# Optimization experiments

Measured on AMD Instinct MI355X. Metric: run time of the kernel, lower is better.

Reference implementation:

```python
import jax, jax.numpy as jnp
import numpy as np
import math

WINDOW_SIZE = 1024
CAUSAL = True


def setup_inputs() -> dict:
    key = jax.random.key(0)
    kq, kk, kv = jax.random.split(key, 3)
    B, H, L, D = 2, 16, 4096, 128
    q = jax.random.normal(kq, (B, H, L, D), dtype=jnp.float32)
    k = jax.random.normal(kk, (B, H, L, D), dtype=jnp.float32)
    v = jax.random.normal(kv, (B, H, L, D), dtype=jnp.float32)
    return {"q": q, "k": k, "v": v}


def _sliding_window_attention(q, k, v):
    # Faithful port of SlidingWindowAttention._blockwise_attention (L > 2048 path).
    B, H, L, D = q.shape
    block = min(WINDOW_SIZE, 1024)
    scale = 1.0 / math.sqrt(D)
    half_w = WINDOW_SIZE // 2
    outs = []
    # Python loop over a small fixed number of blocks (L/block = 4), not data dims.
    for s in range(0, L, block):
        e = min(s + block, L)
        ks = max(0, s - half_w)
        ke = min(L, e + half_w)
        if CAUSAL:
            ke = min(ke, e)
        qb = q[:, :, s:e, :]          # [B,H,Q,D]
        kb = k[:, :, ks:ke, :]        # [B,H,K,D]
        vb = v[:, :, ks:ke, :]        # [B,H,K,D]
        scores = jnp.einsum('bhqd,bhkd->bhqk', qb, kb) * scale
        if CAUSAL:
            qi = jnp.arange(s, e)[:, None]   # [Q,1]
            ki = jnp.arange(ks, ke)[None, :]  # [1,K]
            causal_mask = qi >= ki            # [Q,K]
            scores = jnp.where(causal_mask[None, None], scores, -jnp.inf)
        attn = jax.nn.softmax(scores, axis=-1)
        outs.append(jnp.einsum('bhqk,bhkd->bhqd', attn, vb))
    return jnp.concatenate(outs, axis=2)


def reference(q, k, v):
    return _sliding_window_attention(q, k, v)
```

## Files before the change

### kernel.cpp

```cpp
#include <hip/hip_runtime.h>
#include <hip/hip_bf16.h>

typedef __bf16 bf16_t;
typedef __bf16 bf16x8 __attribute__((ext_vector_type(8)));
typedef __bf16 bf16x4 __attribute__((ext_vector_type(4)));
typedef float f32x4 __attribute__((ext_vector_type(4)));

#define L_SEQ 4096
#define D_DIM 128
#define QT 64
#define KT 64
#define LDK 136
#define LDV 72
#define LDP 72

__global__ __launch_bounds__(256, 2)
void swa_fwd(const float* __restrict__ Qg,
             const float* __restrict__ Kg,
             const float* __restrict__ Vg,
             float* __restrict__ Og) {
    __shared__ __align__(16) bf16_t Kt[KT][LDK];
    __shared__ __align__(16) bf16_t Vt[D_DIM][LDV];
    __shared__ __align__(16) bf16_t Pst[4][16][LDP];

    const int t    = threadIdx.x;
    const int w    = t >> 6;
    const int ln   = t & 15;
    const int quad = (t & 63) >> 4;

    const int id = blockIdx.x;
    const int bh = id & 31;
    const int g  = id >> 5;
    const int q0 = g & 7;
    const int kk = g >> 3;
    const int qt = 16 * (kk >> 1) + ((kk & 1) ? (15 - q0) : q0);

    const size_t base = (size_t)bh * L_SEQ * D_DIM;
    const float* Qp = Qg + base;
    const float* Kp = Kg + base;
    const float* Vp = Vg + base;
    float*       Op = Og + base;

    const int qbase  = qt * QT;
    const int blk    = qbase & ~1023;
    const int kstart = (blk - 512) > 0 ? (blk - 512) : 0;
    const int kend   = qbase + QT;
    const int ntile  = (kend - kstart) / KT;

    const int qw = qbase + w * 16;

    const float SC  = 0.08838834764831845f * 1.4426950408889634f;
    const float FIX = 8.0f;

    bf16x8 qf[4];
    {
        const float* qrow = Qp + (size_t)(qw + ln) * D_DIM + quad * 8;
        #pragma unroll
        for (int ks = 0; ks < 4; ++ks) {
            f32x4 a = *(const f32x4*)(qrow + ks * 32);
            f32x4 b = *(const f32x4*)(qrow + ks * 32 + 4);
            bf16x8 q8;
            #pragma unroll
            for (int j = 0; j < 4; ++j) {
                q8[j]     = (bf16_t)(a[j] * SC);
                q8[4 + j] = (bf16_t)(b[j] * SC);
            }
            qf[ks] = q8;
        }
    }

    f32x4 Oacc[8];
    #pragma unroll
    for (int dt = 0; dt < 8; ++dt) Oacc[dt] = f32x4{0.f, 0.f, 0.f, 0.f};
    float lsum[4] = {0.f, 0.f, 0.f, 0.f};
    const float NEG = -1.0e30f;

    const int kr   = t >> 5;
    const int kc   = t & 31;
    const int vd   = t & 127;
    const int vkcb = t >> 7;

    f32x4 kreg[8];
    float vreg[4][8];

    auto load_tile = [&](int k0) {
        #pragma unroll
        for (int i = 0; i < 8; ++i)
            kreg[i] = *(const f32x4*)(Kp + (size_t)(k0 + kr + 8 * i) * D_DIM + kc * 4);
        #pragma unroll
        for (int r2 = 0; r2 < 4; ++r2) {
            const int kcc = vkcb + 2 * r2;
            #pragma unroll
            for (int j = 0; j < 8; ++j)
                vreg[r2][j] = Vp[(size_t)(k0 + kcc * 8 + j) * D_DIM + vd];
        }
    };
    auto store_tile = [&]() {
        #pragma unroll
        for (int i = 0; i < 8; ++i) {
            bf16x4 h;
            #pragma unroll
            for (int j = 0; j < 4; ++j) h[j] = (bf16_t)kreg[i][j];
            *(bf16x4*)(&Kt[kr + 8 * i][kc * 4]) = h;
        }
        #pragma unroll
        for (int r2 = 0; r2 < 4; ++r2) {
            const int kcc = vkcb + 2 * r2;
            bf16x8 h8;
            #pragma unroll
            for (int j = 0; j < 8; ++j) h8[j] = (bf16_t)vreg[r2][j];
            *(bf16x8*)(&Vt[vd][kcc * 8]) = h8;
        }
    };

    load_tile(kstart);

    for (int kt = 0; kt < ntile; ++kt) {
        const int k0 = kstart + kt * KT;
        __syncthreads();
        store_tile();
        __syncthreads();
        if (kt + 1 < ntile) load_tile(k0 + KT);

        f32x4 S[4];
        #pragma unroll
        for (int nt = 0; nt < 4; ++nt) S[nt] = f32x4{0.f, 0.f, 0.f, 0.f};
        #pragma unroll
        for (int ks = 0; ks < 4; ++ks) {
            #pragma unroll
            for (int nt = 0; nt < 4; ++nt) {
                bf16x8 bk = *(const bf16x8*)(&Kt[nt * 16 + ln][quad * 8 + ks * 32]);
                S[nt] = __builtin_amdgcn_mfma_f32_16x16x32_bf16(qf[ks], bk, S[nt], 0, 0, 0);
            }
        }

        const bool lastTile = (kt == ntile - 1);
        float p[4][4];
        #pragma unroll
        for (int nt = 0; nt < 4; ++nt) {
            #pragma unroll
            for (int r = 0; r < 4; ++r) {
                float s = S[nt][r];
                if (lastTile) {
                    const int kg = k0 + nt * 16 + ln;
                    const int qg = qw + quad * 4 + r;
                    if (kg > qg) s = NEG;
                }
                const float e = __builtin_amdgcn_exp2f(s - FIX);
                p[nt][r] = e;
                lsum[r] += e;
            }
        }

        #pragma unroll
        for (int nt = 0; nt < 4; ++nt)
            #pragma unroll
            for (int r = 0; r < 4; ++r)
                Pst[w][quad * 4 + r][nt * 16 + ln] = (bf16_t)p[nt][r];

        bf16x8 pa[2];
        #pragma unroll
        for (int ks2 = 0; ks2 < 2; ++ks2)
            pa[ks2] = *(const bf16x8*)(&Pst[w][ln][quad * 8 + ks2 * 32]);

        #pragma unroll
        for (int dt = 0; dt < 8; ++dt) {
            #pragma unroll
            for (int ks2 = 0; ks2 < 2; ++ks2) {
                bf16x8 bv = *(const bf16x8*)(&Vt[dt * 16 + ln][quad * 8 + ks2 * 32]);
                Oacc[dt] = __builtin_amdgcn_mfma_f32_16x16x32_bf16(pa[ks2], bv, Oacc[dt], 0, 0, 0);
            }
        }
    }

    #pragma unroll
    for (int r = 0; r < 4; ++r) {
        float l = lsum[r];
        #pragma unroll
        for (int msk = 1; msk < 16; msk <<= 1)
            l += __shfl_xor(l, msk, 64);
        const float inv = (l > 0.f) ? (1.f / l) : 0.f;
        const int qg = qw + quad * 4 + r;
        float* orow = Op + (size_t)qg * D_DIM + ln;
        #pragma unroll
        for (int dt = 0; dt < 8; ++dt)
            orow[dt * 16] = Oacc[dt][r] * inv;
    }
}

extern "C" void kernel_launch(void* const* d_in, const int* in_sizes, int n_in,
                              void* d_out, int out_size, void* d_ws, size_t ws_size,
                              hipStream_t stream) {
    const float* q = (const float*)d_in[0];
    const float* k = (const float*)d_in[1];
    const float* v = (const float*)d_in[2];
    float* o = (float*)d_out;
    dim3 grid(2048);
    dim3 block(256);
    swa_fwd<<<grid, block, 0, stream>>>(q, k, v, o);
}
```

Before: 298.9 us.

## Pre-convert K/V to swizzled bf16 workspace and stream tiles via async LDS loads

Adds two pre-pass kernels that convert K to bf16 and V to a transposed bf16 layout per 64-key block, both XOR-swizzled, in the workspace. The main kernel then double-buffers K/V tiles into shared memory with global_load_lds, handles 128 queries per block with two MFMA row tiles per wave, and writes output as vectorized float4. This removes the per-tile fp32-to-bf16 conversion, the register staging and the scattered V loads, and halves K/V reloads per query. In exchange it adds extra global traffic and two launches for the conversion passes, and falls back to the old kernel if the workspace is too small.

```diff
diff --git a/kernel.cpp b/kernel.cpp
--- a/kernel.cpp
+++ b/kernel.cpp
@@ -1,5 +1,6 @@
 #include <hip/hip_runtime.h>
 #include <hip/hip_bf16.h>
+#include <stdint.h>
 
 typedef __bf16 bf16_t;
 typedef __bf16 bf16x8 __attribute__((ext_vector_type(8)));
@@ -8,8 +9,213 @@
 
 #define L_SEQ 4096
 #define D_DIM 128
+#define NBH   32
+#define KT    64
+
+__global__ __launch_bounds__(256)
+void cvt_k(const float* __restrict__ Kg, bf16_t* __restrict__ Kws) {
+    const int n   = blockIdx.x * 256 + threadIdx.x;
+    const int key = n >> 4;
+    const int pc  = n & 15;
+    const int lc  = pc ^ (key & 7);
+    const float* s = Kg + (size_t)key * D_DIM + lc * 8;
+    f32x4 a = *(const f32x4*)(s);
+    f32x4 b = *(const f32x4*)(s + 4);
+    bf16x8 h;
+    #pragma unroll
+    for (int j = 0; j < 4; ++j) { h[j] = (bf16_t)a[j]; h[4 + j] = (bf16_t)b[j]; }
+    *(bf16x8*)(Kws + (size_t)key * D_DIM + pc * 8) = h;
+}
+
+__global__ __launch_bounds__(256)
+void cvt_v(const float* __restrict__ Vg, bf16_t* __restrict__ Vws) {
+    const int blk  = blockIdx.x;
+    const int bh   = blk >> 6;
+    const int kb   = blk & 63;
+    const int t    = threadIdx.x;
+    const int d    = t & 127;
+    const int half = t >> 7;
+    const float* src0 = Vg + (size_t)(bh * L_SEQ + kb * 64) * D_DIM + d;
+    bf16_t* dstrow = Vws + ((size_t)(bh * 64 + kb) * D_DIM + d) * 64;
+    #pragma unroll
+    for (int r2 = 0; r2 < 4; ++r2) {
+        const int lc = half + 2 * r2;
+        bf16x8 h;
+        #pragma unroll
+        for (int j = 0; j < 8; ++j)
+            h[j] = (bf16_t)src0[(size_t)(lc * 8 + j) * D_DIM];
+        const int pc = lc ^ (d & 7);
+        *(bf16x8*)(&dstrow[pc * 8]) = h;
+    }
+}
+
+__device__ __forceinline__ void ld_lds16(const void* g, void* s) {
+    __builtin_amdgcn_global_load_lds(
+        (const __attribute__((address_space(1))) unsigned int*)g,
+        (__attribute__((address_space(3))) unsigned int*)s, 16, 0, 0);
+}
+
+#define QT2 128
+
+__global__ __launch_bounds__(256, 2)
+void swa_fwd2(const float* __restrict__ Qg,
+              const bf16_t* __restrict__ Kws,
+              const bf16_t* __restrict__ Vws,
+              float* __restrict__ Og) {
+    __shared__ __align__(16) bf16_t KtS[2][KT * D_DIM];
+    __shared__ __align__(16) bf16_t VtS[2][D_DIM * KT];
+    __shared__ __align__(16) bf16_t Pst[4][16 * KT];
+
+    const int t    = threadIdx.x;
+    const int w    = t >> 6;
+    const int ln   = t & 15;
+    const int quad = (t & 63) >> 4;
+    const int l7   = t & 7;
+
+    const int id = blockIdx.x;
+    const int bh = id & 31;
+    const int g  = id >> 5;
+    const int r_ = g & 7;
+    const int k_ = g >> 3;
+    const int qt = 8 * k_ + ((k_ & 1) ? (7 - r_) : r_);
+
+    const size_t baseF = (size_t)bh * L_SEQ * D_DIM;
+    const float*  Qp = Qg + baseF;
+    float*        Op = Og + baseF;
+    const bf16_t* Kb = Kws + baseF;
+    const bf16_t* Vb = Vws + (size_t)bh * 64 * D_DIM * 64;
+
+    const int qbase  = qt * QT2;
+    const int blk    = qbase & ~1023;
+    const int kstart = (blk - 512) > 0 ? (blk - 512) : 0;
+    const int kend   = qbase + QT2;
+    const int ntile  = (kend - kstart) / KT;
+
+    const float SC  = 0.08838834764831845f * 1.4426950408889634f;
+    const float FIX = 8.0f;
+    const float NEG = -1.0e30f;
+
+    bf16x8 qf[2][4];
+    #pragma unroll
+    for (int mt = 0; mt < 2; ++mt) {
+        const float* qrow = Qp + (size_t)(qbase + w * 32 + mt * 16 + ln) * D_DIM + quad * 8;
+        #pragma unroll
+        for (int ks = 0; ks < 4; ++ks) {
+            f32x4 a = *(const f32x4*)(qrow + ks * 32);
+            f32x4 b = *(const f32x4*)(qrow + ks * 32 + 4);
+            bf16x8 q8;
+            #pragma unroll
+            for (int j = 0; j < 4; ++j) { q8[j] = (bf16_t)(a[j] * SC); q8[4 + j] = (bf16_t)(b[j] * SC); }
+            qf[mt][ks] = q8;
+        }
+    }
+
+    f32x4 Oacc[2][8];
+    #pragma unroll
+    for (int mt = 0; mt < 2; ++mt)
+        #pragma unroll
+        for (int dt = 0; dt < 8; ++dt) Oacc[mt][dt] = f32x4{0.f, 0.f, 0.f, 0.f};
+    float lsum[2] = {0.f, 0.f};
+
+    auto stage = [&](int b, int k0) {
+        const char* ksrc = (const char*)Kb + (size_t)k0 * 256;
+        const char* vsrc = (const char*)Vb + (size_t)(k0 >> 6) * 16384;
+        char* kd = (char*)(&KtS[b][0]);
+        char* vd = (char*)(&VtS[b][0]);
+        #pragma unroll
+        for (int i = 0; i < 4; ++i) {
+            const int off = (i * 256 + t) * 16;
+            ld_lds16(ksrc + off, kd + off);
+            ld_lds16(vsrc + off, vd + off);
+        }
+    };
+
+    stage(0, kstart);
+    __syncthreads();
+
+    int buf = 0;
+    for (int kt = 0; kt < ntile; ++kt) {
+        const int k0 = kstart + kt * KT;
+        if (kt + 1 < ntile) stage(buf ^ 1, k0 + KT);
+
+        f32x4 S[2][4];
+        #pragma unroll
+        for (int mt = 0; mt < 2; ++mt)
+            #pragma unroll
+            for (int nt = 0; nt < 4; ++nt) S[mt][nt] = f32x4{0.f, 0.f, 0.f, 0.f};
+        #pragma unroll
+        for (int ks = 0; ks < 4; ++ks) {
+            #pragma unroll
+            for (int nt = 0; nt < 4; ++nt) {
+                const bf16x8 bk = *(const bf16x8*)(
+                    &KtS[buf][(nt * 16 + ln) * D_DIM + (((quad + ks * 4) ^ l7) * 8)]);
+                S[0][nt] = __builtin_amdgcn_mfma_f32_16x16x32_bf16(bk, qf[0][ks], S[0][nt], 0, 0, 0);
+                S[1][nt] = __builtin_amdgcn_mfma_f32_16x16x32_bf16(bk, qf[1][ks], S[1][nt], 0, 0, 0);
+            }
+        }
+
+        bf16x8 pa[2][2];
+        #pragma unroll
+        for (int mt = 0; mt < 2; ++mt) {
+            const int qwm = qbase + w * 32 + mt * 16;
+            const int qg  = qwm + ln;
+            const bool nm = (k0 + KT - 1) > qwm;
+            #pragma unroll
+            for (int nt = 0; nt < 4; ++nt) {
+                bf16x4 hp;
+                #pragma unroll
+                for (int r = 0; r < 4; ++r) {
+                    float s = S[mt][nt][r];
+                    if (nm) {
+                        const int kg = k0 + nt * 16 + quad * 4 + r;
+                        if (kg > qg) s = NEG;
+                    }
+                    const float e = __builtin_amdgcn_exp2f(s - FIX);
+                    lsum[mt] += e;
+                    hp[r] = (bf16_t)e;
+                }
+                *(bf16x4*)(&Pst[w][ln * 64 + (((nt * 2 + (quad >> 1)) ^ l7) * 8) + (quad & 1) * 4]) = hp;
+            }
+            #pragma unroll
+            for (int ks2 = 0; ks2 < 2; ++ks2)
+                pa[mt][ks2] = *(const bf16x8*)(
+                    &Pst[w][ln * 64 + (((quad + ks2 * 4) ^ l7) * 8)]);
+        }
+
+        #pragma unroll
+        for (int dt = 0; dt < 8; ++dt) {
+            #pragma unroll
+            for (int ks2 = 0; ks2 < 2; ++ks2) {
+                const bf16x8 bv = *(const bf16x8*)(
+                    &VtS[buf][(dt * 16 + ln) * 64 + (((quad + ks2 * 4) ^ l7) * 8)]);
+                Oacc[0][dt] = __builtin_amdgcn_mfma_f32_16x16x32_bf16(bv, pa[0][ks2], Oacc[0][dt], 0, 0, 0);
+                Oacc[1][dt] = __builtin_amdgcn_mfma_f32_16x16x32_bf16(bv, pa[1][ks2], Oacc[1][dt], 0, 0, 0);
+            }
+        }
+
+        __syncthreads();
+        buf ^= 1;
+    }
+
+    #pragma unroll
+    for (int mt = 0; mt < 2; ++mt) {
+        float l = lsum[mt];
+        l += __shfl_xor(l, 16, 64);
+        l += __shfl_xor(l, 32, 64);
+        const float inv = (l > 0.f) ? (1.f / l) : 0.f;
+        const int qg = qbase + w * 32 + mt * 16 + ln;
+        float* orow = Op + (size_t)qg * D_DIM + quad * 4;
+        #pragma unroll
+        for (int dt = 0; dt < 8; ++dt) {
+            f32x4 o = Oacc[mt][dt];
+            #pragma unroll
+            for (int j = 0; j < 4; ++j) o[j] *= inv;
+            *(f32x4*)(orow + dt * 16) = o;
+        }
+    }
+}
+
 #define QT 64
-#define KT 64
 #define LDK 136
 #define LDV 72
 #define LDP 72
@@ -21,7 +227,7 @@
              float* __restrict__ Og) {
     __shared__ __align__(16) bf16_t Kt[KT][LDK];
     __shared__ __align__(16) bf16_t Vt[D_DIM][LDV];
-    __shared__ __align__(16) bf16_t Pst[4][16][LDP];
+    __shared__ __align__(16) bf16_t Pstf[4][16][LDP];
 
     const int t    = threadIdx.x;
     const int w    = t >> 6;
@@ -156,12 +362,12 @@
         for (int nt = 0; nt < 4; ++nt)
             #pragma unroll
             for (int r = 0; r < 4; ++r)
-                Pst[w][quad * 4 + r][nt * 16 + ln] = (bf16_t)p[nt][r];
+                Pstf[w][quad * 4 + r][nt * 16 + ln] = (bf16_t)p[nt][r];
 
         bf16x8 pa[2];
         #pragma unroll
         for (int ks2 = 0; ks2 < 2; ++ks2)
-            pa[ks2] = *(const bf16x8*)(&Pst[w][ln][quad * 8 + ks2 * 32]);
+            pa[ks2] = *(const bf16x8*)(&Pstf[w][ln][quad * 8 + ks2 * 32]);
 
         #pragma unroll
         for (int dt = 0; dt < 8; ++dt) {
@@ -195,7 +401,15 @@
     const float* k = (const float*)d_in[1];
     const float* v = (const float*)d_in[2];
     float* o = (float*)d_out;
-    dim3 grid(2048);
-    dim3 block(256);
-    swa_fwd<<<grid, block, 0, stream>>>(q, k, v, o);
-}
+
+    const size_t kbytes = (size_t)NBH * L_SEQ * D_DIM * sizeof(bf16_t);
+    if (d_ws && ws_size >= 2 * kbytes) {
+        bf16_t* kws = (bf16_t*)d_ws;
+        bf16_t* vws = (bf16_t*)((char*)d_ws + kbytes);
+        cvt_k<<<dim3(8192), dim3(256), 0, stream>>>(k, kws);
+        cvt_v<<<dim3(2048), dim3(256), 0, stream>>>(v, vws);
+        swa_fwd2<<<dim3(1024), dim3(256), 0, stream>>>(q, kws, vws, o);
+    } else {
+        swa_fwd<<<dim3(2048), dim3(256), 0, stream>>>(q, k, v, o);
+    }
+}
```

After: 306.8 us. 2.6% more time.
